# Performance work log

Measured on AMD Instinct MI355X. Metric: run time of the kernel, lower is better.

Reference implementation:

```python
import jax, jax.numpy as jnp
import numpy as np


def setup_inputs() -> dict:
    key = jax.random.key(0)
    k1, k2 = jax.random.split(key)
    H, D, N = 1, 256, 65536        # (heads=1, embedding_dim, num_tokens)
    C = 1024                       # num_embeddings (codebook size)
    inputs = jax.random.normal(k1, (H, D, N), dtype=jnp.float32)
    embedding = jax.random.normal(k2, (H, C, D), dtype=jnp.float32)
    return {"inputs": inputs, "embedding": embedding}


COMMITMENT_COST = 0.25


def reference(inputs, embedding):
    # inputs: (h, d, n) -> flat: (h, n, d)
    flat = jnp.transpose(inputs, (0, 2, 1))
    # negative euclidean distance (matches -torch.cdist, p=2)
    x2 = jnp.sum(flat * flat, axis=-1, keepdims=True)            # (h, n, 1)
    e2 = jnp.sum(embedding * embedding, axis=-1)[:, None, :]     # (h, 1, c)
    xe = jnp.einsum('hnd,hcd->hnc', flat, embedding)             # (h, n, c)
    d2 = jnp.maximum(x2 + e2 - 2.0 * xe, 0.0)
    distances = -jnp.sqrt(d2)                                    # (h, n, c)
    encoding_indices = jnp.argmax(distances, axis=2)             # (h, n)
    # gather codebook vectors: h == 1
    quantized = jnp.take(embedding[0], encoding_indices[0], axis=0)[None]  # (h, n, d)
    commit_loss = jnp.mean((jax.lax.stop_gradient(quantized) - flat) ** 2)
    loss = COMMITMENT_COST * commit_loss
    # straight-through estimator
    quantized_st = flat + jax.lax.stop_gradient(quantized - flat)
    out = jnp.transpose(quantized_st, (0, 2, 1))                 # (h, d, n)
    return out, encoding_indices, loss, distances
```

## Files before the change

kernel.cpp:

```cpp
#include <hip/hip_runtime.h>
#include <math.h>

#define N_TOK 65536
#define D_DIM 256
#define C_NUM 1024

#define OUT_OFF   0
#define IDX_OFF   (D_DIM * N_TOK)
#define LOSS_OFF  (IDX_OFF + N_TOK)
#define DIST_OFF  (LOSS_OFF + 1)

#define MARGIN 0.01f
#define NPART 4096

typedef __attribute__((ext_vector_type(8))) short bf16x8;
typedef __attribute__((ext_vector_type(4))) float f32x4;

static __device__ __forceinline__ unsigned short f2bf(float f) {
  unsigned int u = __float_as_uint(f);
  unsigned int r = (u + 0x7fffu + ((u >> 16) & 1u)) >> 16;
  return (unsigned short)r;
}
static __device__ __forceinline__ float bf2f(unsigned short h) {
  return __uint_as_float(((unsigned int)h) << 16);
}


#define WS_EH   0
#define WS_EL   524288
#define WS_E2   1048576
#define WS_PART 1052672
#define WS_TP   1069056
#define WS_NEEDED (WS_TP + (size_t)N_TOK * 16 * 4)

#define XH_OFF_F 0
#define XL_OFF_F 8388608

#define PART_OFF_F 263168

__global__ __launch_bounds__(256) void kA2_prep(const float* __restrict__ X,
                                                const float* __restrict__ E,
                                                float* __restrict__ out,
                                                unsigned char* __restrict__ ws) {
  const int bid = blockIdx.x, tid = threadIdx.x;
  if (bid < 1024) {
    unsigned short* XhG = (unsigned short*)(out + XH_OFF_F);
    unsigned short* XlG = (unsigned short*)(out + XL_OFF_F);
    const int n = bid * 64 + (tid >> 2);
    const int sg = (tid & 3) * 16;
    unsigned short* xh = XhG + (size_t)n * D_DIM;
    unsigned short* xl = XlG + (size_t)n * D_DIM;
    float s = 0.0f;
#pragma unroll 1
    for (int dc = 0; dc < D_DIM; dc += 64) {
      float v[16];
#pragma unroll
      for (int j = 0; j < 16; ++j) v[j] = X[(size_t)(dc + sg + j) * N_TOK + n];
      unsigned short hh[16], ll[16];
#pragma unroll
      for (int j = 0; j < 16; ++j) {
        s = fmaf(v[j], v[j], s);
        hh[j] = f2bf(v[j]);
        ll[j] = f2bf(v[j] - bf2f(hh[j]));
      }
      *(bf16x8*)(xh + dc + sg) = *(bf16x8*)&hh[0];
      *(bf16x8*)(xh + dc + sg + 8) = *(bf16x8*)&hh[8];
      *(bf16x8*)(xl + dc + sg) = *(bf16x8*)&ll[0];
      *(bf16x8*)(xl + dc + sg + 8) = *(bf16x8*)&ll[8];
    }
    s += __shfl_xor(s, 1, 64);
    s += __shfl_xor(s, 2, 64);
    if ((tid & 3) == 0) out[IDX_OFF + n] = s;
  } else {
    unsigned short* EhG = (unsigned short*)(ws + WS_EH);
    unsigned short* ElG = (unsigned short*)(ws + WS_EL);
    float* e2p = (float*)(ws + WS_E2);
    const int lane = tid & 63, w = tid >> 6;
#pragma unroll 1
    for (int cc = 0; cc < 16; ++cc) {
      const int c = (bid - 1024) * 64 + w * 16 + cc;
      const float4 v = *(const float4*)(E + (size_t)c * D_DIM + lane * 4);
      unsigned short h0 = f2bf(v.x), h1 = f2bf(v.y), h2 = f2bf(v.z), h3 = f2bf(v.w);
      unsigned short l0 = f2bf(v.x - bf2f(h0)), l1 = f2bf(v.y - bf2f(h1));
      unsigned short l2 = f2bf(v.z - bf2f(h2)), l3 = f2bf(v.w - bf2f(h3));
      ushort4 hv = make_ushort4(h0, h1, h2, h3);
      ushort4 lv = make_ushort4(l0, l1, l2, l3);
      *(ushort4*)(EhG + (size_t)c * D_DIM + lane * 4) = hv;
      *(ushort4*)(ElG + (size_t)c * D_DIM + lane * 4) = lv;
      float s = v.x * v.x + v.y * v.y + v.z * v.z + v.w * v.w;
#pragma unroll
      for (int off = 32; off; off >>= 1) s += __shfl_down(s, off, 64);
      if (lane == 0) e2p[c] = s;
    }
  }
}

#define TM 64
#define TC 256
#define BK 32
#define XS2 264

__global__ __launch_bounds__(256) void k2c_dist(float* __restrict__ out,
                                                unsigned char* __restrict__ ws) {
  __shared__ __align__(16) unsigned short xh[TM * XS2];
  __shared__ __align__(16) unsigned short xl[TM * XS2];

  const unsigned short* __restrict__ XhG = (const unsigned short*)(out + XH_OFF_F);
  const unsigned short* __restrict__ XlG = (const unsigned short*)(out + XL_OFF_F);
  const unsigned short* __restrict__ EhG = (const unsigned short*)(ws + WS_EH);
  const float* __restrict__ e2p = (const float*)(ws + WS_E2);
  float* __restrict__ tpv = (float*)(ws + WS_TP);

  const int tid = threadIdx.x;
  const int lane = tid & 63, wave = tid >> 6;

  const int bid = blockIdx.x;
  const int xcd = bid & 7;
  const int slot = bid >> 3;
  const int bx = slot & 3;
  const int by = xcd * 128 + (slot >> 2);
  const int c0 = bx * TC;
  const int n0 = by * TM;

  const int wc = c0 + wave * 64;
  const int m = lane & 15;
  const int q = lane >> 4;

  {
    const int tl = tid >> 2;
    const int seg = (tid & 3) * 64;
    const unsigned short* gh = XhG + (size_t)(n0 + tl) * D_DIM + seg;
    const unsigned short* gl = XlG + (size_t)(n0 + tl) * D_DIM + seg;
    unsigned short* sh = xh + tl * XS2 + seg;
    unsigned short* sl = xl + tl * XS2 + seg;
#pragma unroll
    for (int j = 0; j < 8; ++j) {
      *(bf16x8*)(sh + j * 8) = *(const bf16x8*)(gh + j * 8);
      *(bf16x8*)(sl + j * 8) = *(const bf16x8*)(gl + j * 8);
    }
  }

  float x2r[16];
#pragma unroll
  for (int i = 0; i < 4; ++i)
#pragma unroll
    for (int r = 0; r < 4; ++r)
      x2r[i * 4 + r] = out[IDX_OFF + n0 + i * 16 + q * 4 + r];
  float e2v[4];
#pragma unroll
  for (int t = 0; t < 4; ++t) e2v[t] = e2p[wc + t * 16 + m];

  __syncthreads();

  f32x4 acc[4][4];
#pragma unroll
  for (int i = 0; i < 4; ++i)
#pragma unroll
    for (int t = 0; t < 4; ++t) acc[i][t] = (f32x4){0.f, 0.f, 0.f, 0.f};

  const unsigned short* bp[4];
#pragma unroll
  for (int t = 0; t < 4; ++t) bp[t] = EhG + (size_t)(wc + t * 16 + m) * D_DIM + q * 8;
  const size_t loEu = (size_t)(WS_EL - WS_EH) / 2;

#pragma unroll 2
  for (int kb = 0; kb < D_DIM; kb += BK) {
    bf16x8 ah[4], al[4], bh[4], bl[4];
#pragma unroll
    for (int t = 0; t < 4; ++t) {
      bh[t] = *(const bf16x8*)(bp[t] + kb);
      bl[t] = *(const bf16x8*)(bp[t] + loEu + kb);
    }
#pragma unroll
    for (int i = 0; i < 4; ++i) {
      const int ro = (i * 16 + m) * XS2 + kb + q * 8;
      ah[i] = *(const bf16x8*)&xh[ro];
      al[i] = *(const bf16x8*)&xl[ro];
    }
#pragma unroll
    for (int i = 0; i < 4; ++i)
#pragma unroll
      for (int t = 0; t < 4; ++t) {
        acc[i][t] = __builtin_amdgcn_mfma_f32_16x16x32_bf16(ah[i], bh[t], acc[i][t], 0, 0, 0);
        acc[i][t] = __builtin_amdgcn_mfma_f32_16x16x32_bf16(ah[i], bl[t], acc[i][t], 0, 0, 0);
        acc[i][t] = __builtin_amdgcn_mfma_f32_16x16x32_bf16(al[i], bh[t], acc[i][t], 0, 0, 0);
      }
  }

#pragma unroll
  for (int i = 0; i < 4; ++i) {
#pragma unroll
    for (int r = 0; r < 4; ++r) {
      const int tok = n0 + i * 16 + q * 4 + r;
      const float x2v = x2r[i * 4 + r];
      const size_t row = DIST_OFF + (size_t)tok * C_NUM;
      float bestv = -3.4e38f;
#pragma unroll
      for (int t = 0; t < 4; ++t) {
        float d2 = fmaf(-2.0f, acc[i][t][r], x2v + e2v[t]);
        d2 = fmaxf(d2, 0.0f);
        const float dd = -sqrtf(d2);
        out[row + wc + t * 16 + m] = dd;
        bestv = fmaxf(bestv, dd);
      }
#pragma unroll
      for (int off = 1; off < 16; off <<= 1)
        bestv = fmaxf(bestv, __shfl_xor(bestv, off, 64));
      if ((lane & 15) == 0)
        tpv[(size_t)tok * 16 + bx * 4 + wave] = bestv;
    }
  }
}

__global__ __launch_bounds__(256) void k3a4_argmax(const float* __restrict__ X,
                                                   const float* __restrict__ E,
                                                   float* __restrict__ out,
                                                   unsigned char* __restrict__ ws) {
  const float* __restrict__ tpv = (const float*)(ws + WS_TP);
  float* __restrict__ part = (float*)(ws + WS_PART);
  __shared__ float lsum[4];
  const int tid = threadIdx.x, lane = tid & 63, w = tid >> 6;
  const int g = lane & 15, seg = lane >> 4;
  const int n = blockIdx.x * 16 + w * 4 + seg;

  const float gval = tpv[(size_t)n * 16 + g];
  float best = gval;
#pragma unroll
  for (int off = 1; off < 16; off <<= 1)
    best = fmaxf(best, __shfl_xor(best, off, 64));
  const float thr = best - MARGIN;
  const unsigned long long bal = __ballot(gval > thr);
  const unsigned m16 = (unsigned)((bal >> (seg * 16)) & 0xffffull);
  const int nflag = __popc(m16);
  const int j = __ffs(m16) - 1;

  const float4 rv =
      *(const float4*)(out + DIST_OFF + (size_t)n * C_NUM + j * 64 + g * 4);

  float bv = rv.x;
  int bix = j * 64 + g * 4;
  if (rv.y > bv) { bv = rv.y; bix = j * 64 + g * 4 + 1; }
  if (rv.z > bv) { bv = rv.z; bix = j * 64 + g * 4 + 2; }
  if (rv.w > bv) { bv = rv.w; bix = j * 64 + g * 4 + 3; }
  int cnt = (rv.x > thr ? 1 : 0) + (rv.y > thr ? 1 : 0) +
            (rv.z > thr ? 1 : 0) + (rv.w > thr ? 1 : 0);
#pragma unroll
  for (int off = 1; off < 16; off <<= 1) {
    const float ov = __shfl_xor(bv, off, 64);
    const int oi = __shfl_xor(bix, off, 64);
    cnt += __shfl_xor(cnt, off, 64);
    if (ov > bv || (ov == bv && oi < bix)) { bv = ov; bix = oi; }
  }

  const bool fast = (nflag == 1) && (cnt == 1);
  float lval = 0.0f;
  if (fast && g == 0) {
    out[IDX_OFF + n] = (float)bix;
    lval = bv * bv;
  }

  unsigned long long smask = __ballot((!fast) && (g == 0));
  float sloss = 0.0f;
  while (smask) {
    const int sl = __ffsll((long long)smask) - 1;
    smask &= smask - 1;
    const int nn = blockIdx.x * 16 + w * 4 + (sl >> 4);
    {
      const float* row = out + DIST_OFF + (size_t)nn * C_NUM;
      float v[16];
      float bestf = -3.4e38f;
      int bif = 0x7fffffff;
#pragma unroll
      for (int jj = 0; jj < 16; ++jj) {
        v[jj] = row[jj * 64 + lane];
        if (v[jj] > bestf) { bestf = v[jj]; bif = jj * 64 + lane; }
      }
#pragma unroll
      for (int off = 32; off; off >>= 1) {
        const float ov = __shfl_xor(bestf, off, 64);
        const int oi = __shfl_xor(bif, off, 64);
        if (ov > bestf || (ov == bestf && oi < bif)) { bestf = ov; bif = oi; }
      }
      const float thrf = bestf - MARGIN;
      unsigned long long masks[16];
      int total = 0;
#pragma unroll
      for (int jj = 0; jj < 16; ++jj) {
        masks[jj] = __ballot(v[jj] > thrf);
        total += __popcll(masks[jj]);
      }
      float best_d2 = bestf * bestf;
      int best_idx = bif;
      if (total > 1) {
        best_d2 = 3.4e38f;
        best_idx = 0x7fffffff;
        for (int jj = 0; jj < 16; ++jj) {
          unsigned long long mm = masks[jj];
          while (mm) {
            const int l = __ffsll((long long)mm) - 1;
            mm &= mm - 1;
            const int c = jj * 64 + l;
            float sx = 0.f, se = 0.f, sxe = 0.f;
#pragma unroll
            for (int r = 0; r < 4; ++r) {
              const int d = r * 64 + lane;
              const float xv = X[(size_t)d * N_TOK + nn];
              const float ev = E[(size_t)c * D_DIM + d];
              sx = fmaf(xv, xv, sx);
              se = fmaf(ev, ev, se);
              sxe = fmaf(xv, ev, sxe);
            }
            float d2 = fmaf(-2.f, sxe, sx + se);
#pragma unroll
            for (int off = 32; off; off >>= 1) d2 += __shfl_xor(d2, off, 64);
            d2 = fmaxf(d2, 0.f);
            if (d2 < best_d2 || (d2 == best_d2 && c < best_idx)) {
              best_d2 = d2; best_idx = c;
            }
          }
        }
      }
      if (lane == 0) {
        out[IDX_OFF + nn] = (float)best_idx;
        sloss += best_d2;
      }
    }
  }

  float wl = lval + ((lane == 0) ? sloss : 0.0f);
#pragma unroll
  for (int off = 32; off; off >>= 1) wl += __shfl_down(wl, off, 64);
  if (lane == 0) lsum[w] = wl;
  __syncthreads();
  if (tid == 0)
    part[blockIdx.x] = lsum[0] + lsum[1] + lsum[2] + lsum[3];
}

__global__ __launch_bounds__(256) void k3b2_loss(float* __restrict__ out,
                                                 unsigned char* __restrict__ ws) {
  const float* __restrict__ part = (const float*)(ws + WS_PART);
  __shared__ float red[4];
  const int tid = threadIdx.x, lane = tid & 63, w = tid >> 6;
  float s = 0.0f;
#pragma unroll
  for (int i = 0; i < NPART / 256; ++i) s += part[i * 256 + tid];
#pragma unroll
  for (int off = 32; off; off >>= 1) s += __shfl_down(s, off, 64);
  if (lane == 0) red[w] = s;
  __syncthreads();
  if (tid == 0)
    out[LOSS_OFF] = (red[0] + red[1] + red[2] + red[3]) *
                    (0.25f / ((float)N_TOK * (float)D_DIM));
}

#define EH_OFF_F  0
#define EL_OFF_F  131072
#define E2_OFF_F  262144

__global__ __launch_bounds__(256) void kA_prep(const float* __restrict__ X,
                                               const float* __restrict__ E,
                                               float* __restrict__ out) {
  const int bid = blockIdx.x, tid = threadIdx.x;
  if (bid < 256) {
    const int n = bid * 256 + tid;
    float s = 0.0f;
#pragma unroll 8
    for (int d = 0; d < D_DIM; ++d) {
      float v = X[(size_t)d * N_TOK + n];
      s = fmaf(v, v, s);
    }
    out[IDX_OFF + n] = s;
  } else {
    unsigned short* EhG = (unsigned short*)(out + EH_OFF_F);
    unsigned short* ElG = (unsigned short*)(out + EL_OFF_F);
    const int lane = tid & 63, w = tid >> 6;
#pragma unroll 1
    for (int cc = 0; cc < 16; ++cc) {
      const int c = (bid - 256) * 64 + w * 16 + cc;
      const float4 v = *(const float4*)(E + (size_t)c * D_DIM + lane * 4);
      unsigned short h0 = f2bf(v.x), h1 = f2bf(v.y), h2 = f2bf(v.z), h3 = f2bf(v.w);
      unsigned short l0 = f2bf(v.x - bf2f(h0)), l1 = f2bf(v.y - bf2f(h1));
      unsigned short l2 = f2bf(v.z - bf2f(h2)), l3 = f2bf(v.w - bf2f(h3));
      ushort4 hv = make_ushort4(h0, h1, h2, h3);
      ushort4 lv = make_ushort4(l0, l1, l2, l3);
      *(ushort4*)(EhG + (size_t)c * D_DIM + lane * 4) = hv;
      *(ushort4*)(ElG + (size_t)c * D_DIM + lane * 4) = lv;
      float s = v.x * v.x + v.y * v.y + v.z * v.z + v.w * v.w;
#pragma unroll
      for (int off = 32; off; off >>= 1) s += __shfl_down(s, off, 64);
      if (lane == 0) out[E2_OFF_F + c] = s;
    }
  }
}

#define XS 40

__global__ __launch_bounds__(256) void k2_dist(const float* __restrict__ X,
                                               float* __restrict__ out) {
  __shared__ __align__(16) unsigned short xhb[2][TM * XS];
  __shared__ __align__(16) unsigned short xlb[2][TM * XS];

  const unsigned short* __restrict__ EhG = (const unsigned short*)(out + EH_OFF_F);
  const unsigned short* __restrict__ ElG = (const unsigned short*)(out + EL_OFF_F);

  const int tid = threadIdx.x;
  const int lane = tid & 63, wave = tid >> 6;
  const int bid = blockIdx.x;
  const int xcd = bid & 7;
  const int slot = bid >> 3;
  const int bx = slot & 3;
  const int by = xcd * 128 + (slot >> 2);
  const int c0 = bx * TC;
  const int n0 = by * TM;

  const int wc = c0 + wave * 64;
  const int m = lane & 15;
  const int q = lane >> 4;

  f32x4 acc[4][4];
#pragma unroll
  for (int i = 0; i < 4; ++i)
#pragma unroll
    for (int t = 0; t < 4; ++t) acc[i][t] = (f32x4){0.f, 0.f, 0.f, 0.f};

  const int sn = lane;
  const int kg = wave;

  float xv[8];
  {
    const float* xp = X + (size_t)(kg * 8) * N_TOK + n0 + sn;
#pragma unroll
    for (int j = 0; j < 8; ++j) xv[j] = xp[(size_t)j * N_TOK];
  }

#pragma unroll 1
  for (int kb = 0; kb < D_DIM; kb += BK) {
    const int p = (kb >> 5) & 1;
    bf16x8 bh[4], bl[4];
#pragma unroll
    for (int t = 0; t < 4; ++t) {
      const size_t eoff = (size_t)(wc + t * 16 + m) * D_DIM + kb + q * 8;
      bh[t] = *(const bf16x8*)(EhG + eoff);
      bl[t] = *(const bf16x8*)(ElG + eoff);
    }
    unsigned short hh[8], ll[8];
#pragma unroll
    for (int j = 0; j < 8; ++j) {
      hh[j] = f2bf(xv[j]);
      ll[j] = f2bf(xv[j] - bf2f(hh[j]));
    }
    *(bf16x8*)&xhb[p][sn * XS + kg * 8] = *(bf16x8*)hh;
    *(bf16x8*)&xlb[p][sn * XS + kg * 8] = *(bf16x8*)ll;
    if (kb + BK < D_DIM) {
      const float* xp = X + (size_t)(kb + BK + kg * 8) * N_TOK + n0 + sn;
#pragma unroll
      for (int j = 0; j < 8; ++j) xv[j] = xp[(size_t)j * N_TOK];
    }
    __syncthreads();
    bf16x8 ah[4], al[4];
#pragma unroll
    for (int i = 0; i < 4; ++i) {
      const int ro = (i * 16 + m) * XS + q * 8;
      ah[i] = *(const bf16x8*)&xhb[p][ro];
      al[i] = *(const bf16x8*)&xlb[p][ro];
    }
#pragma unroll
    for (int i = 0; i < 4; ++i)
#pragma unroll
      for (int t = 0; t < 4; ++t) {
        acc[i][t] = __builtin_amdgcn_mfma_f32_16x16x32_bf16(ah[i], bh[t], acc[i][t], 0, 0, 0);
        acc[i][t] = __builtin_amdgcn_mfma_f32_16x16x32_bf16(ah[i], bl[t], acc[i][t], 0, 0, 0);
        acc[i][t] = __builtin_amdgcn_mfma_f32_16x16x32_bf16(al[i], bh[t], acc[i][t], 0, 0, 0);
      }
  }

  float e2v[4];
#pragma unroll
  for (int t = 0; t < 4; ++t) e2v[t] = out[E2_OFF_F + wc + t * 16 + m];

#pragma unroll
  for (int i = 0; i < 4; ++i) {
#pragma unroll
    for (int r = 0; r < 4; ++r) {
      const int tok = n0 + i * 16 + q * 4 + r;
      const float x2v = out[IDX_OFF + tok];
      const size_t row = DIST_OFF + (size_t)tok * C_NUM;
#pragma unroll
      for (int t = 0; t < 4; ++t) {
        float d2 = fmaf(-2.0f, acc[i][t][r], x2v + e2v[t]);
        d2 = fmaxf(d2, 0.0f);
        out[row + wc + t * 16 + m] = -sqrtf(d2);
      }
    }
  }
}

__global__ __launch_bounds__(256) void k3_argmax(const float* __restrict__ X,
                                                 const float* __restrict__ E,
                                                 float* __restrict__ out) {
  __shared__ float lsum[4];
  const int tid = threadIdx.x, lane = tid & 63, w = tid >> 6;
  float wloss = 0.0f;

#pragma unroll 1
  for (int it = 0; it < 4; ++it) {
    const int n = blockIdx.x * 16 + w * 4 + it;
    const float* row = out + DIST_OFF + (size_t)n * C_NUM;

    float v[16];
    float best = -3.4e38f;
    int bi = 0x7fffffff;
#pragma unroll
    for (int j = 0; j < 16; ++j) {
      v[j] = row[j * 64 + lane];
      if (v[j] > best) { best = v[j]; bi = j * 64 + lane; }
    }
#pragma unroll
    for (int off = 32; off; off >>= 1) {
      const float ov = __shfl_xor(best, off, 64);
      const int oi = __shfl_xor(bi, off, 64);
      if (ov > best || (ov == best && oi < bi)) { best = ov; bi = oi; }
    }
    const float thr = best - MARGIN;
    unsigned long long masks[16];
    int total = 0;
#pragma unroll
    for (int j = 0; j < 16; ++j) {
      masks[j] = __ballot(v[j] > thr);
      total += __popcll(masks[j]);
    }
    float best_d2 = best * best;
    int best_idx = bi;
    if (total > 1) {
      best_d2 = 3.4e38f;
      best_idx = 0x7fffffff;
      for (int j = 0; j < 16; ++j) {
        unsigned long long mm = masks[j];
        while (mm) {
          const int l = __ffsll((long long)mm) - 1;
          mm &= mm - 1;
          const int c = j * 64 + l;
          float sx = 0.f, se = 0.f, sxe = 0.f;
#pragma unroll
          for (int r = 0; r < 4; ++r) {
            const int d = r * 64 + lane;
            const float xv = X[(size_t)d * N_TOK + n];
            const float ev = E[(size_t)c * D_DIM + d];
            sx = fmaf(xv, xv, sx);
            se = fmaf(ev, ev, se);
            sxe = fmaf(xv, ev, sxe);
          }
          float d2 = fmaf(-2.f, sxe, sx + se);
#pragma unroll
          for (int off = 32; off; off >>= 1) d2 += __shfl_xor(d2, off, 64);
          d2 = fmaxf(d2, 0.f);
          if (d2 < best_d2 || (d2 == best_d2 && c < best_idx)) {
            best_d2 = d2; best_idx = c;
          }
        }
      }
    }
    if (lane == 0) out[IDX_OFF + n] = (float)best_idx;
    wloss += best_d2;
  }
  if (lane == 0) lsum[w] = wloss;
  __syncthreads();
  if (tid == 0)
    out[PART_OFF_F + blockIdx.x] = lsum[0] + lsum[1] + lsum[2] + lsum[3];
}

__global__ __launch_bounds__(256) void k3b_loss(float* __restrict__ out) {
  __shared__ float red[4];
  const int tid = threadIdx.x, lane = tid & 63, w = tid >> 6;
  float s = 0.0f;
#pragma unroll
  for (int i = 0; i < NPART / 256; ++i) s += out[PART_OFF_F + i * 256 + tid];
#pragma unroll
  for (int off = 32; off; off >>= 1) s += __shfl_down(s, off, 64);
  if (lane == 0) red[w] = s;
  __syncthreads();
  if (tid == 0)
    out[LOSS_OFF] = (red[0] + red[1] + red[2] + red[3]) *
                    (0.25f / ((float)N_TOK * (float)D_DIM));
}

__global__ __launch_bounds__(256) void k4_gather(const float* __restrict__ E,
                                                 float* __restrict__ out) {
  const int g = blockIdx.x * 256 + threadIdx.x;
  const int n = g * 4;
  const float4 iv = *(const float4*)&out[IDX_OFF + n];
  const int i0 = (int)iv.x;
  const int i1 = (int)iv.y;
  const int i2 = (int)iv.z;
  const int i3 = (int)iv.w;
  const float* e0 = E + (size_t)i0 * D_DIM;
  const float* e1 = E + (size_t)i1 * D_DIM;
  const float* e2 = E + (size_t)i2 * D_DIM;
  const float* e3 = E + (size_t)i3 * D_DIM;
  const int d0 = blockIdx.y * 32;
#pragma unroll 4
  for (int d = d0; d < d0 + 32; ++d) {
    float4 wv = make_float4(e0[d], e1[d], e2[d], e3[d]);
    *(float4*)&out[(size_t)d * N_TOK + n] = wv;
  }
}

extern "C" void kernel_launch(void* const* d_in, const int* in_sizes, int n_in,
                              void* d_out, int out_size, void* d_ws, size_t ws_size,
                              hipStream_t stream) {
  const float* X = (const float*)d_in[0];
  const float* E = (const float*)d_in[1];
  float* out = (float*)d_out;

  if (ws_size >= WS_NEEDED && d_ws != nullptr) {
    unsigned char* ws = (unsigned char*)d_ws;
    hipLaunchKernelGGL(kA2_prep, dim3(1040), dim3(256), 0, stream, X, E, out, ws);
    hipLaunchKernelGGL(k2c_dist, dim3((C_NUM / TC) * (N_TOK / TM)), dim3(256), 0,
                       stream, out, ws);
    hipLaunchKernelGGL(k3a4_argmax, dim3(N_TOK / 16), dim3(256), 0, stream,
                       X, E, out, ws);
    hipLaunchKernelGGL(k3b2_loss, dim3(1), dim3(256), 0, stream, out, ws);
    hipLaunchKernelGGL(k4_gather, dim3(N_TOK / 4 / 256, 8), dim3(256), 0, stream,
                       E, out);
  } else {
    hipLaunchKernelGGL(kA_prep, dim3(272), dim3(256), 0, stream, X, E, out);
    hipLaunchKernelGGL(k2_dist, dim3((C_NUM / TC) * (N_TOK / TM)), dim3(256), 0,
                       stream, X, out);
    hipLaunchKernelGGL(k3_argmax, dim3(N_TOK / 16), dim3(256), 0, stream, X, E, out);
    hipLaunchKernelGGL(k3b_loss, dim3(1), dim3(256), 0, stream, out);
    hipLaunchKernelGGL(k4_gather, dim3(N_TOK / 4 / 256, 8), dim3(256), 0, stream,
                       E, out);
  }
}
```

Baseline: 614.4 us.

## Coalesce prep transpose via LDS, vectorize gather loads, raise MFMA priority

The prep kernel now reads X with lanes mapped to consecutive tokens so global loads coalesce, then transposes through an LDS tile before writing the bf16 hi/lo rows. The token norm is reduced through shared memory. The distance kernel unrolls its k-loop further and raises wave priority around the MFMA block. The gather kernel reads codebook rows with float4 loads and transposes them in registers. The cost is extra LDS use and two barriers per chunk in prep, plus higher register pressure from the larger unroll.

```diff
diff --git a/kernel.cpp b/kernel.cpp
--- a/kernel.cpp
+++ b/kernel.cpp
@@ -38,39 +38,65 @@
 
 #define PART_OFF_F 263168
 
+#define TS 72
+
 __global__ __launch_bounds__(256) void kA2_prep(const float* __restrict__ X,
                                                 const float* __restrict__ E,
                                                 float* __restrict__ out,
                                                 unsigned char* __restrict__ ws) {
   const int bid = blockIdx.x, tid = threadIdx.x;
   if (bid < 1024) {
+    __shared__ __align__(16) unsigned short lh[64 * TS];
+    __shared__ __align__(16) unsigned short ll[64 * TS];
+    __shared__ float xs2[4][64];
+
     unsigned short* XhG = (unsigned short*)(out + XH_OFF_F);
     unsigned short* XlG = (unsigned short*)(out + XL_OFF_F);
-    const int n = bid * 64 + (tid >> 2);
+    const int lane = tid & 63, w = tid >> 6;
+    const int n0 = bid * 64;
+    const int tl = tid >> 2;
     const int sg = (tid & 3) * 16;
-    unsigned short* xh = XhG + (size_t)n * D_DIM;
-    unsigned short* xl = XlG + (size_t)n * D_DIM;
+
     float s = 0.0f;
 #pragma unroll 1
     for (int dc = 0; dc < D_DIM; dc += 64) {
       float v[16];
 #pragma unroll
-      for (int j = 0; j < 16; ++j) v[j] = X[(size_t)(dc + sg + j) * N_TOK + n];
-      unsigned short hh[16], ll[16];
+      for (int j = 0; j < 16; ++j)
+        v[j] = X[(size_t)(dc + w * 16 + j) * N_TOK + n0 + lane];
+      unsigned short hh[16], llv[16];
 #pragma unroll
       for (int j = 0; j < 16; ++j) {
         s = fmaf(v[j], v[j], s);
         hh[j] = f2bf(v[j]);
-        ll[j] = f2bf(v[j] - bf2f(hh[j]));
-      }
-      *(bf16x8*)(xh + dc + sg) = *(bf16x8*)&hh[0];
-      *(bf16x8*)(xh + dc + sg + 8) = *(bf16x8*)&hh[8];
-      *(bf16x8*)(xl + dc + sg) = *(bf16x8*)&ll[0];
-      *(bf16x8*)(xl + dc + sg + 8) = *(bf16x8*)&ll[8];
-    }
-    s += __shfl_xor(s, 1, 64);
-    s += __shfl_xor(s, 2, 64);
-    if ((tid & 3) == 0) out[IDX_OFF + n] = s;
+        llv[j] = f2bf(v[j] - bf2f(hh[j]));
+      }
+      *(bf16x8*)&lh[lane * TS + w * 16] = *(bf16x8*)&hh[0];
+      *(bf16x8*)&lh[lane * TS + w * 16 + 8] = *(bf16x8*)&hh[8];
+      *(bf16x8*)&ll[lane * TS + w * 16] = *(bf16x8*)&llv[0];
+      *(bf16x8*)&ll[lane * TS + w * 16 + 8] = *(bf16x8*)&llv[8];
+      __syncthreads();
+      {
+        const bf16x8 h0 = *(const bf16x8*)&lh[tl * TS + sg];
+        const bf16x8 h1 = *(const bf16x8*)&lh[tl * TS + sg + 8];
+        const bf16x8 l0 = *(const bf16x8*)&ll[tl * TS + sg];
+        const bf16x8 l1 = *(const bf16x8*)&ll[tl * TS + sg + 8];
+        unsigned short* gh = XhG + (size_t)(n0 + tl) * D_DIM + dc + sg;
+        unsigned short* gl = XlG + (size_t)(n0 + tl) * D_DIM + dc + sg;
+        *(bf16x8*)gh = h0;
+        *(bf16x8*)(gh + 8) = h1;
+        *(bf16x8*)gl = l0;
+        *(bf16x8*)(gl + 8) = l1;
+      }
+      __syncthreads();
+    }
+    xs2[w][lane] = s;
+    __syncthreads();
+    if (w == 0) {
+      const float t2 = (xs2[0][lane] + xs2[1][lane]) +
+                       (xs2[2][lane] + xs2[3][lane]);
+      out[IDX_OFF + n0 + lane] = t2;
+    }
   } else {
     unsigned short* EhG = (unsigned short*)(ws + WS_EH);
     unsigned short* ElG = (unsigned short*)(ws + WS_EL);
@@ -163,7 +189,7 @@
   for (int t = 0; t < 4; ++t) bp[t] = EhG + (size_t)(wc + t * 16 + m) * D_DIM + q * 8;
   const size_t loEu = (size_t)(WS_EL - WS_EH) / 2;
 
-#pragma unroll 2
+#pragma unroll 4
   for (int kb = 0; kb < D_DIM; kb += BK) {
     bf16x8 ah[4], al[4], bh[4], bl[4];
 #pragma unroll
@@ -177,6 +203,7 @@
       ah[i] = *(const bf16x8*)&xh[ro];
       al[i] = *(const bf16x8*)&xl[ro];
     }
+    __builtin_amdgcn_s_setprio(1);
 #pragma unroll
     for (int i = 0; i < 4; ++i)
 #pragma unroll
@@ -185,6 +212,7 @@
         acc[i][t] = __builtin_amdgcn_mfma_f32_16x16x32_bf16(ah[i], bl[t], acc[i][t], 0, 0, 0);
         acc[i][t] = __builtin_amdgcn_mfma_f32_16x16x32_bf16(al[i], bh[t], acc[i][t], 0, 0, 0);
       }
+    __builtin_amdgcn_s_setprio(0);
   }
 
 #pragma unroll
@@ -598,10 +626,16 @@
   const float* e2 = E + (size_t)i2 * D_DIM;
   const float* e3 = E + (size_t)i3 * D_DIM;
   const int d0 = blockIdx.y * 32;
-#pragma unroll 4
-  for (int d = d0; d < d0 + 32; ++d) {
-    float4 wv = make_float4(e0[d], e1[d], e2[d], e3[d]);
-    *(float4*)&out[(size_t)d * N_TOK + n] = wv;
+#pragma unroll
+  for (int dd = 0; dd < 32; dd += 4) {
+    const float4 a0 = *(const float4*)&e0[d0 + dd];
+    const float4 a1 = *(const float4*)&e1[d0 + dd];
+    const float4 a2 = *(const float4*)&e2[d0 + dd];
+    const float4 a3 = *(const float4*)&e3[d0 + dd];
+    *(float4*)&out[(size_t)(d0 + dd + 0) * N_TOK + n] = make_float4(a0.x, a1.x, a2.x, a3.x);
+    *(float4*)&out[(size_t)(d0 + dd + 1) * N_TOK + n] = make_float4(a0.y, a1.y, a2.y, a3.y);
+    *(float4*)&out[(size_t)(d0 + dd + 2) * N_TOK + n] = make_float4(a0.z, a1.z, a2.z, a3.z);
+    *(float4*)&out[(size_t)(d0 + dd + 3) * N_TOK + n] = make_float4(a0.w, a1.w, a2.w, a3.w);
   }
 }
 
```

Result: faster. 590.7 us (-3.9%).
